# Kernel tuning notes

Hardware: AMD Instinct MI355X
Metric: run time of the kernel (lower is better)

The kernel has to match this reference:

```python
import jax, jax.numpy as jnp
import numpy as np

B, S, D = 32, 4096, 256

def setup_inputs() -> dict:
    key = jax.random.key(0)
    k1, k2, k3 = jax.random.split(key, 3)
    inputs = jax.random.normal(k1, (B, S, D), dtype=jnp.float32)
    W = jax.random.normal(k2, (D, D), dtype=jnp.float32) * 0.05  # 'random_normal' init
    b = jnp.zeros((D,), dtype=jnp.float32)
    V = jax.random.normal(k3, (D, 1), dtype=jnp.float32) * 0.05
    return {"inputs": inputs, "W": W, "b": b, "V": V}

def reference(inputs, W, b, V):
    # score: [B,S,D] = tanh(inputs @ W + b)
    score = jnp.tanh(jnp.einsum('bsd,de->bse', inputs, W) + b)
    # logits: [B,S,1]; softmax over seq axis (axis=1)
    logits = jnp.einsum('bsd,do->bso', score, V)
    attn = jax.nn.softmax(logits, axis=1)            # [B,S,1]
    # weighted sum pooling over seq -> [B,D]
    context = jnp.sum(attn * inputs, axis=1)
    return context
```

## Files before the change

### kernel.cpp

```cpp
#include <hip/hip_runtime.h>
#include <hip/hip_bf16.h>

#define DD 256
#define SS 4096

typedef __bf16 bf16x8 __attribute__((ext_vector_type(8)));
typedef float  f32x4  __attribute__((ext_vector_type(4)));

__device__ __forceinline__ float fast_tanh(float x) {
  float e = __expf(2.0f * x);
  return 1.0f - 2.0f / (e + 1.0f);
}

template<int CTRL>
__device__ __forceinline__ float dpp_mov(float v) {
  return __int_as_float(__builtin_amdgcn_update_dpp(0, __float_as_int(v), CTRL, 0xF, 0xF, true));
}
__device__ __forceinline__ float row16_sum(float v) {
  v += dpp_mov<0xB1>(v);
  v += dpp_mov<0x4E>(v);
  v += dpp_mov<0x124>(v);
  v += dpp_mov<0x128>(v);
  return v;
}
__device__ __forceinline__ float row16_max(float v) {
  v = fmaxf(v, dpp_mov<0xB1>(v));
  v = fmaxf(v, dpp_mov<0x4E>(v));
  v = fmaxf(v, dpp_mov<0x124>(v));
  v = fmaxf(v, dpp_mov<0x128>(v));
  return v;
}

__global__ __launch_bounds__(256) void prep_kernel(
    const float* __restrict__ W, __bf16* __restrict__ WF)
{
  const int c = blockIdx.x * 256 + threadIdx.x;
  const int lane_c = c & 63;
  const int ks  = (c >> 6) & 7;
  const int n0  = c >> 9;
  const int col = n0 * 16 + (lane_c & 15);
  const int k0  = ks * 32 + (lane_c >> 4) * 8;
  const float* wp = W + k0 * DD + col;
  bf16x8 fr;
  #pragma unroll
  for (int i = 0; i < 8; ++i) fr[i] = (__bf16)wp[i * DD];
  *reinterpret_cast<bf16x8*>(WF + (size_t)c * 8) = fr;
}

#define LOADB(buf, n0q) { \
  const bf16x8* _src = WFv + ((n0q) * 8 * 64 + lane); \
  _Pragma("unroll") \
  for (int _ks = 0; _ks < 8; ++_ks) buf[_ks] = _src[_ks * 64]; }

#define COMPUTE(buf, n0q) { \
  f32x4 _acc0 = {0.f,0.f,0.f,0.f}; \
  f32x4 _acc1 = {0.f,0.f,0.f,0.f}; \
  _Pragma("unroll") \
  for (int _ks = 0; _ks < 8; ++_ks) { \
    _acc0 = __builtin_amdgcn_mfma_f32_16x16x32_bf16(a[0][_ks], buf[_ks], _acc0, 0, 0, 0); \
    _acc1 = __builtin_amdgcn_mfma_f32_16x16x32_bf16(a[1][_ks], buf[_ks], _acc1, 0, 0, 0); } \
  const int _col = (n0q) * 16 + lg; \
  const float _vc = Vs[_col], _bc = Bs[_col]; \
  _Pragma("unroll") \
  for (int _r = 0; _r < 4; ++_r) { \
    sp0[_r] += fast_tanh(_acc0[_r] + _bc) * _vc; \
    sp1[_r] += fast_tanh(_acc1[_r] + _bc) * _vc; } }

__global__ __launch_bounds__(512, 4) void fused_kernel(
    const float* __restrict__ X, const __bf16* __restrict__ WF,
    const float* __restrict__ bias, const float* __restrict__ V,
    float* __restrict__ Pout, float* __restrict__ Mout, float* __restrict__ Sout)
{
  __shared__ float Pacc[8][DD];
  __shared__ float Vs[DD];
  __shared__ float Bs[DD];
  __shared__ float wred[8];
  __shared__ float sred[8];

  const int t = threadIdx.x;
  if (t < DD) { Vs[t] = V[t]; Bs[t] = bias[t]; }
  __syncthreads();

  const int wave = t >> 6, lane = t & 63;
  const int g  = lane >> 4;
  const int lg = lane & 15;
  const size_t rowBase = (size_t)blockIdx.x * 256 + (size_t)wave * 32;
  const bf16x8* WFv = reinterpret_cast<const bf16x8*>(WF);

  bf16x8 a[2][8];
  #pragma unroll
  for (int st = 0; st < 2; ++st) {
    const float* xr = X + (rowBase + st * 16 + lg) * DD;
    #pragma unroll
    for (int ks = 0; ks < 8; ++ks) {
      const float4* p = reinterpret_cast<const float4*>(xr + ks * 32 + g * 8);
      float4 f0 = p[0], f1 = p[1];
      bf16x8 fr;
      fr[0] = (__bf16)f0.x; fr[1] = (__bf16)f0.y; fr[2] = (__bf16)f0.z; fr[3] = (__bf16)f0.w;
      fr[4] = (__bf16)f1.x; fr[5] = (__bf16)f1.y; fr[6] = (__bf16)f1.z; fr[7] = (__bf16)f1.w;
      a[st][ks] = fr;
    }
  }

  float sp0[4] = {0.f,0.f,0.f,0.f};
  float sp1[4] = {0.f,0.f,0.f,0.f};
  bf16x8 bufA[8], bufB[8];
  LOADB(bufA, 0);
  #pragma unroll
  for (int n2 = 0; n2 < 8; ++n2) {
    LOADB(bufB, n2 * 2 + 1);
    COMPUTE(bufA, n2 * 2);
    if (n2 < 7) LOADB(bufA, n2 * 2 + 2);
    COMPUTE(bufB, n2 * 2 + 1);
  }

  #pragma unroll
  for (int r = 0; r < 4; ++r) { sp0[r] = row16_sum(sp0[r]); sp1[r] = row16_sum(sp1[r]); }

  const int src = ((lg >> 2) << 4) | lg;
  float l0 = 0.f, l1 = 0.f;
  #pragma unroll
  for (int r = 0; r < 4; ++r) {
    float v0 = __shfl(sp0[r], src, 64);
    float v1 = __shfl(sp1[r], src, 64);
    if ((lg & 3) == r) { l0 = v0; l1 = v1; }
  }

  float wm = row16_max(fmaxf(l0, l1));
  if (lane == 0) wred[wave] = wm;
  __syncthreads();
  float M = -1e30f;
  #pragma unroll
  for (int w = 0; w < 8; ++w) M = fmaxf(M, wred[w]);

  const float w0 = __expf(l0 - M);
  const float w1 = __expf(l1 - M);

  float se = row16_sum(w0 + w1);
  if (lane == 0) sred[wave] = se;

  #pragma unroll
  for (int ks = 0; ks < 8; ++ks) {
    float p8[8];
    #pragma unroll
    for (int i = 0; i < 8; ++i)
      p8[i] = w0 * (float)a[0][ks][i] + w1 * (float)a[1][ks][i];
    #pragma unroll
    for (int i = 0; i < 8; ++i) p8[i] = row16_sum(p8[i]);
    if (lg < 2) {
      float4 v = (lg == 0) ? make_float4(p8[0], p8[1], p8[2], p8[3])
                           : make_float4(p8[4], p8[5], p8[6], p8[7]);
      *reinterpret_cast<float4*>(&Pacc[wave][ks * 32 + g * 8 + lg * 4]) = v;
    }
  }
  __syncthreads();

  if (t < DD) {
    float s = 0.f;
    #pragma unroll
    for (int w = 0; w < 8; ++w) s += Pacc[w][t];
    Pout[(size_t)blockIdx.x * DD + t] = s;
  }
  if (t == 0) {
    float ss = 0.f;
    #pragma unroll
    for (int w = 0; w < 8; ++w) ss += sred[w];
    Sout[blockIdx.x] = ss;
    Mout[blockIdx.x] = M;
  }
}

__global__ __launch_bounds__(256) void combine_kernel(
    const float* __restrict__ P, const float* __restrict__ Mb,
    const float* __restrict__ Sb, float* __restrict__ ctx)
{
  const int b = blockIdx.x, t = threadIdx.x;
  float Mg = -1e30f;
  #pragma unroll
  for (int k = 0; k < 16; ++k) Mg = fmaxf(Mg, Mb[b * 16 + k]);
  float denom = 0.f, acc = 0.f;
  #pragma unroll
  for (int k = 0; k < 16; ++k) {
    const float f = __expf(Mb[b * 16 + k] - Mg);
    denom += f * Sb[b * 16 + k];
    acc   += f * P[(size_t)(b * 16 + k) * DD + t];
  }
  ctx[b * DD + t] = acc / denom;
}

extern "C" void kernel_launch(void* const* d_in, const int* in_sizes, int n_in,
                              void* d_out, int out_size, void* d_ws, size_t ws_size,
                              hipStream_t stream) {
  const float* X    = (const float*)d_in[0];
  const float* W    = (const float*)d_in[1];
  const float* bias = (const float*)d_in[2];
  const float* V    = (const float*)d_in[3];
  float* ctx = (float*)d_out;

  __bf16* WF = (__bf16*)d_ws;
  float* P = (float*)((char*)d_ws + 128 * 1024);
  float* M = P + 512 * DD;
  float* S = M + 512;

  prep_kernel<<<32, 256, 0, stream>>>(W, WF);
  fused_kernel<<<512, 512, 0, stream>>>(X, WF, bias, V, P, M, S);
  combine_kernel<<<32, 256, 0, stream>>>(P, M, S, ctx);
}
```

Measured before the change: 57.54 us.

## Shrink fused blocks to 4 waves of 16 rows with per-wave softmax

The fused kernel now uses 2048 blocks of 256 threads, and each wave handles 16 rows instead of 32. The block-wide max barrier is replaced by per-wave max and sum that are rescaled in the block epilogue, and the combine step merges 64 partials per batch. The W fragments are no longer double-buffered and V/bias are read straight from global memory inside a non-unrolled loop, so fewer registers are used and more waves can be resident. The cost is that each W fragment is reused across half as many rows, so B-operand load traffic doubles and less latency is hidden within a wave.

```diff
diff --git a/kernel.cpp b/kernel.cpp
--- a/kernel.cpp
+++ b/kernel.cpp
@@ -47,50 +47,25 @@
   *reinterpret_cast<bf16x8*>(WF + (size_t)c * 8) = fr;
 }
 
-#define LOADB(buf, n0q) { \
-  const bf16x8* _src = WFv + ((n0q) * 8 * 64 + lane); \
-  _Pragma("unroll") \
-  for (int _ks = 0; _ks < 8; ++_ks) buf[_ks] = _src[_ks * 64]; }
-
-#define COMPUTE(buf, n0q) { \
-  f32x4 _acc0 = {0.f,0.f,0.f,0.f}; \
-  f32x4 _acc1 = {0.f,0.f,0.f,0.f}; \
-  _Pragma("unroll") \
-  for (int _ks = 0; _ks < 8; ++_ks) { \
-    _acc0 = __builtin_amdgcn_mfma_f32_16x16x32_bf16(a[0][_ks], buf[_ks], _acc0, 0, 0, 0); \
-    _acc1 = __builtin_amdgcn_mfma_f32_16x16x32_bf16(a[1][_ks], buf[_ks], _acc1, 0, 0, 0); } \
-  const int _col = (n0q) * 16 + lg; \
-  const float _vc = Vs[_col], _bc = Bs[_col]; \
-  _Pragma("unroll") \
-  for (int _r = 0; _r < 4; ++_r) { \
-    sp0[_r] += fast_tanh(_acc0[_r] + _bc) * _vc; \
-    sp1[_r] += fast_tanh(_acc1[_r] + _bc) * _vc; } }
-
-__global__ __launch_bounds__(512, 4) void fused_kernel(
+__global__ __launch_bounds__(256, 8) void fused_kernel(
     const float* __restrict__ X, const __bf16* __restrict__ WF,
     const float* __restrict__ bias, const float* __restrict__ V,
     float* __restrict__ Pout, float* __restrict__ Mout, float* __restrict__ Sout)
 {
-  __shared__ float Pacc[8][DD];
-  __shared__ float Vs[DD];
-  __shared__ float Bs[DD];
-  __shared__ float wred[8];
-  __shared__ float sred[8];
+  __shared__ float Pw[4][DD];
+  __shared__ float mw4[4], sw4[4];
 
   const int t = threadIdx.x;
-  if (t < DD) { Vs[t] = V[t]; Bs[t] = bias[t]; }
-  __syncthreads();
-
   const int wave = t >> 6, lane = t & 63;
   const int g  = lane >> 4;
   const int lg = lane & 15;
-  const size_t rowBase = (size_t)blockIdx.x * 256 + (size_t)wave * 32;
+  const int gw = blockIdx.x * 4 + wave;
+  const size_t row = (size_t)gw * 16 + lg;
   const bf16x8* WFv = reinterpret_cast<const bf16x8*>(WF);
 
-  bf16x8 a[2][8];
-  #pragma unroll
-  for (int st = 0; st < 2; ++st) {
-    const float* xr = X + (rowBase + st * 16 + lg) * DD;
+  bf16x8 a[8];
+  {
+    const float* xr = X + row * DD;
     #pragma unroll
     for (int ks = 0; ks < 8; ++ks) {
       const float4* p = reinterpret_cast<const float4*>(xr + ks * 32 + g * 8);
@@ -98,75 +73,66 @@
       bf16x8 fr;
       fr[0] = (__bf16)f0.x; fr[1] = (__bf16)f0.y; fr[2] = (__bf16)f0.z; fr[3] = (__bf16)f0.w;
       fr[4] = (__bf16)f1.x; fr[5] = (__bf16)f1.y; fr[6] = (__bf16)f1.z; fr[7] = (__bf16)f1.w;
-      a[st][ks] = fr;
+      a[ks] = fr;
     }
   }
 
-  float sp0[4] = {0.f,0.f,0.f,0.f};
-  float sp1[4] = {0.f,0.f,0.f,0.f};
-  bf16x8 bufA[8], bufB[8];
-  LOADB(bufA, 0);
-  #pragma unroll
-  for (int n2 = 0; n2 < 8; ++n2) {
-    LOADB(bufB, n2 * 2 + 1);
-    COMPUTE(bufA, n2 * 2);
-    if (n2 < 7) LOADB(bufA, n2 * 2 + 2);
-    COMPUTE(bufB, n2 * 2 + 1);
+  float sp[4] = {0.f, 0.f, 0.f, 0.f};
+  #pragma unroll 1
+  for (int n0 = 0; n0 < 16; ++n0) {
+    const bf16x8* bsrc = WFv + (n0 * 512 + lane);
+    f32x4 acc = {0.f, 0.f, 0.f, 0.f};
+    #pragma unroll
+    for (int ks = 0; ks < 8; ++ks) {
+      bf16x8 bfr = bsrc[ks * 64];
+      acc = __builtin_amdgcn_mfma_f32_16x16x32_bf16(a[ks], bfr, acc, 0, 0, 0);
+    }
+    const int col = n0 * 16 + lg;
+    const float vc = V[col], bc = bias[col];
+    #pragma unroll
+    for (int r = 0; r < 4; ++r)
+      sp[r] += fast_tanh(acc[r] + bc) * vc;
   }
 
   #pragma unroll
-  for (int r = 0; r < 4; ++r) { sp0[r] = row16_sum(sp0[r]); sp1[r] = row16_sum(sp1[r]); }
+  for (int r = 0; r < 4; ++r) sp[r] = row16_sum(sp[r]);
 
   const int src = ((lg >> 2) << 4) | lg;
-  float l0 = 0.f, l1 = 0.f;
+  float l0 = 0.f;
   #pragma unroll
   for (int r = 0; r < 4; ++r) {
-    float v0 = __shfl(sp0[r], src, 64);
-    float v1 = __shfl(sp1[r], src, 64);
-    if ((lg & 3) == r) { l0 = v0; l1 = v1; }
+    float v0 = __shfl(sp[r], src, 64);
+    if ((lg & 3) == r) l0 = v0;
   }
 
-  float wm = row16_max(fmaxf(l0, l1));
-  if (lane == 0) wred[wave] = wm;
-  __syncthreads();
-  float M = -1e30f;
-  #pragma unroll
-  for (int w = 0; w < 8; ++w) M = fmaxf(M, wred[w]);
-
-  const float w0 = __expf(l0 - M);
-  const float w1 = __expf(l1 - M);
-
-  float se = row16_sum(w0 + w1);
-  if (lane == 0) sred[wave] = se;
+  const float m  = row16_max(l0);
+  const float w0 = __expf(l0 - m);
+  const float se = row16_sum(w0);
 
   #pragma unroll
   for (int ks = 0; ks < 8; ++ks) {
     float p8[8];
     #pragma unroll
-    for (int i = 0; i < 8; ++i)
-      p8[i] = w0 * (float)a[0][ks][i] + w1 * (float)a[1][ks][i];
+    for (int i = 0; i < 8; ++i) p8[i] = w0 * (float)a[ks][i];
     #pragma unroll
     for (int i = 0; i < 8; ++i) p8[i] = row16_sum(p8[i]);
     if (lg < 2) {
       float4 v = (lg == 0) ? make_float4(p8[0], p8[1], p8[2], p8[3])
                            : make_float4(p8[4], p8[5], p8[6], p8[7]);
-      *reinterpret_cast<float4*>(&Pacc[wave][ks * 32 + g * 8 + lg * 4]) = v;
+      *reinterpret_cast<float4*>(&Pw[wave][ks * 32 + g * 8 + lg * 4]) = v;
     }
   }
+  if (lane == 0) { mw4[wave] = m; sw4[wave] = se; }
   __syncthreads();
 
-  if (t < DD) {
-    float s = 0.f;
-    #pragma unroll
-    for (int w = 0; w < 8; ++w) s += Pacc[w][t];
-    Pout[(size_t)blockIdx.x * DD + t] = s;
-  }
+  const float Mb = fmaxf(fmaxf(mw4[0], mw4[1]), fmaxf(mw4[2], mw4[3]));
+  const float f0 = __expf(mw4[0] - Mb), f1 = __expf(mw4[1] - Mb);
+  const float f2 = __expf(mw4[2] - Mb), f3 = __expf(mw4[3] - Mb);
+  Pout[(size_t)blockIdx.x * DD + t] =
+      f0 * Pw[0][t] + f1 * Pw[1][t] + f2 * Pw[2][t] + f3 * Pw[3][t];
   if (t == 0) {
-    float ss = 0.f;
-    #pragma unroll
-    for (int w = 0; w < 8; ++w) ss += sred[w];
-    Sout[blockIdx.x] = ss;
-    Mout[blockIdx.x] = M;
+    Sout[blockIdx.x] = f0 * sw4[0] + f1 * sw4[1] + f2 * sw4[2] + f3 * sw4[3];
+    Mout[blockIdx.x] = Mb;
   }
 }
 
@@ -175,17 +141,19 @@
     const float* __restrict__ Sb, float* __restrict__ ctx)
 {
   const int b = blockIdx.x, t = threadIdx.x;
+  const float* Mp = Mb + b * 64;
+  const float* Sp = Sb + b * 64;
   float Mg = -1e30f;
-  #pragma unroll
-  for (int k = 0; k < 16; ++k) Mg = fmaxf(Mg, Mb[b * 16 + k]);
-  float denom = 0.f, acc = 0.f;
-  #pragma unroll
-  for (int k = 0; k < 16; ++k) {
-    const float f = __expf(Mb[b * 16 + k] - Mg);
-    denom += f * Sb[b * 16 + k];
-    acc   += f * P[(size_t)(b * 16 + k) * DD + t];
+  #pragma unroll 8
+  for (int k = 0; k < 64; ++k) Mg = fmaxf(Mg, Mp[k]);
+  float den = 0.f, acc = 0.f;
+  #pragma unroll 4
+  for (int k = 0; k < 64; ++k) {
+    const float f = __expf(Mp[k] - Mg);
+    den += f * Sp[k];
+    acc += f * P[(size_t)(b * 64 + k) * DD + t];
   }
-  ctx[b * DD + t] = acc / denom;
+  ctx[b * DD + t] = acc / den;
 }
 
 extern "C" void kernel_launch(void* const* d_in, const int* in_sizes, int n_in,
@@ -199,10 +167,10 @@
 
   __bf16* WF = (__bf16*)d_ws;
   float* P = (float*)((char*)d_ws + 128 * 1024);
-  float* M = P + 512 * DD;
-  float* S = M + 512;
+  float* M = P + 2048 * DD;
+  float* S = M + 2048;
 
   prep_kernel<<<32, 256, 0, stream>>>(W, WF);
-  fused_kernel<<<512, 512, 0, stream>>>(X, WF, bias, V, P, M, S);
+  fused_kernel<<<2048, 256, 0, stream>>>(X, WF, bias, V, P, M, S);
   combine_kernel<<<32, 256, 0, stream>>>(P, M, S, ctx);
 }
```

Result: slower. 80.15 us (+39.3%).
